# Kernel tuning notes

Measured on AMD Instinct MI355X. Metric: run time of the kernel, lower is better.

The kernel has to match this reference:

```python
import jax, jax.numpy as jnp
import numpy as np

N, D = 4096, 128  # seq length / feature dim of x is N; head dim is D

def setup_inputs() -> dict:
    key = jax.random.key(0)
    k1, k2 = jax.random.split(key)
    x = jax.random.normal(k1, (N, N), dtype=jnp.float32)
    # nn.Linear(N, 3*d): weight [3d, N], bias [3d]; scale weight like torch init
    W = jax.random.normal(k2, (3 * D, N), dtype=jnp.float32) / jnp.sqrt(jnp.float32(N))
    b = jnp.zeros((3 * D,), dtype=jnp.float32)
    return {"x": x, "W": W, "b": b}

def reference(x, W, b):
    # QKV projection: [N, 3d]
    qkv = x @ W.T + b
    Q, K, V = jnp.split(qkv, 3, axis=-1)  # each [N, d]
    # The blockwise online-softmax double loop computes exactly
    # softmax(Q K^T) V with NO 1/sqrt(d) scaling (faithful to source).
    S = Q @ K.T                 # [N, N]
    P = jax.nn.softmax(S, axis=-1)
    return P @ V                # [N, d]
```

## Files before the change

### kernel.cpp

```cpp
#include <hip/hip_runtime.h>
#include <cstdint>
#include <cstddef>

typedef _Float16 f16;
typedef f16 f16x8 __attribute__((ext_vector_type(8)));
typedef f16 f16x4 __attribute__((ext_vector_type(4)));
typedef float f32x4 __attribute__((ext_vector_type(4)));

#define SEQ 4096
#define DH 128
#define QKV_LD 384
#define LOG2E 1.44269504f

__device__ __forceinline__ float fast_exp2(float x) {
#if __has_builtin(__builtin_amdgcn_exp2f)
  return __builtin_amdgcn_exp2f(x);
#else
  return exp2f(x);
#endif
}

__device__ __forceinline__ void gl_lds16(const void* g, void* l) {
  __builtin_amdgcn_global_load_lds((const __attribute__((address_space(1))) void*)g,
                                   (__attribute__((address_space(3))) void*)l, 16, 0, 0);
}

__global__ __launch_bounds__(256) void cvt_kernel(const float4* __restrict__ src,
                                                  f16x4* __restrict__ dst) {
  int i = blockIdx.x * 256 + threadIdx.x;
  float4 v = src[i];
  f16x4 h; h[0] = (f16)v.x; h[1] = (f16)v.y; h[2] = (f16)v.z; h[3] = (f16)v.w;
  dst[i] = h;
}

template <int SPLITS>
__global__ __launch_bounds__(256, 3) void gemm_qkv(const f16* __restrict__ xh,
                                                   const f16* __restrict__ Wh,
                                                   f16* __restrict__ part) {
  __shared__ __align__(16) f16 Ax[128 * 64];
  __shared__ __align__(16) f16 Bx[128 * 64];
  const int m0 = blockIdx.x * 128;
  const int n0 = blockIdx.y * 128;
  const int split = blockIdx.z;
  const int kc = SEQ / SPLITS;
  const int k0 = split * kc;
  const int tid = threadIdx.x;
  const int lane = tid & 63, wave = tid >> 6;
  const int wr = (wave >> 1) * 64, wc = (wave & 1) * 64;
  const int l15 = lane & 15, quad = lane >> 4;

  f32x4 acc[4][4] = {};

  for (int kt = k0; kt < k0 + kc; kt += 64) {
#pragma unroll
    for (int r = 0; r < 4; ++r) {
      int c = r * 256 + tid;
      int row = c >> 3, ch = c & 7;
      gl_lds16(&xh[(size_t)(m0 + row) * SEQ + kt + ((ch ^ (row & 7)) << 3)],
               &Ax[(size_t)c << 3]);
    }
#pragma unroll
    for (int r = 0; r < 4; ++r) {
      int c = r * 256 + tid;
      int row = c >> 3, ch = c & 7;
      gl_lds16(&Wh[(size_t)(n0 + row) * SEQ + kt + ((ch ^ (row & 7)) << 3)],
               &Bx[(size_t)c << 3]);
    }
    __syncthreads();
#pragma unroll
    for (int ks = 0; ks < 2; ++ks) {
      f16x8 a[4], bb[4];
#pragma unroll
      for (int t = 0; t < 4; ++t) {
        int ar = wr + t * 16 + l15;
        int ac = (ks * 4 + quad) ^ (ar & 7);
        a[t] = *(const f16x8*)&Ax[ar * 64 + ac * 8];
        int br = wc + t * 16 + l15;
        int bc = (ks * 4 + quad) ^ (br & 7);
        bb[t] = *(const f16x8*)&Bx[br * 64 + bc * 8];
      }
#pragma unroll
      for (int mt = 0; mt < 4; ++mt)
#pragma unroll
        for (int nt = 0; nt < 4; ++nt)
          acc[mt][nt] = __builtin_amdgcn_mfma_f32_16x16x32_f16(a[mt], bb[nt], acc[mt][nt], 0, 0, 0);
    }
    __syncthreads();
  }

  f16* pw = part + (size_t)split * SEQ * QKV_LD;
#pragma unroll
  for (int mt = 0; mt < 4; ++mt) {
#pragma unroll
    for (int nt = 0; nt < 4; ++nt) {
      int col = n0 + wc + nt * 16 + l15;
      int rowbase = m0 + wr + mt * 16 + quad * 4;
#pragma unroll
      for (int rr = 0; rr < 4; ++rr)
        pw[(size_t)(rowbase + rr) * QKV_LD + col] = (f16)acc[mt][nt][rr];
    }
  }
}

template <int SPLITS>
__global__ __launch_bounds__(256) void reduce_qkv(const f16* __restrict__ part,
                                                  const float* __restrict__ bias,
                                                  f16* __restrict__ qkv) {
  int i = (blockIdx.x * 256 + threadIdx.x) * 8;
  float acc[8] = {};
#pragma unroll
  for (int s = 0; s < SPLITS; ++s) {
    f16x8 p = *(const f16x8*)&part[(size_t)s * SEQ * QKV_LD + i];
#pragma unroll
    for (int j = 0; j < 8; ++j) acc[j] += (float)p[j];
  }
  int col = i % QKV_LD;
  f16x8 o;
#pragma unroll
  for (int j = 0; j < 8; ++j) o[j] = (f16)(acc[j] + bias[col + j]);
  *(f16x8*)&qkv[i] = o;
}

__global__ __launch_bounds__(256) void transpose_v(const f16* __restrict__ qkv,
                                                   f16* __restrict__ Vt) {
  __shared__ __align__(16) f16 T[64][72];
  const int r0 = blockIdx.x * 64;
  const int c0 = blockIdx.y * 64;
  const int tid = threadIdx.x;
#pragma unroll
  for (int rep = 0; rep < 2; ++rep) {
    int idx = rep * 256 + tid;
    int row = idx >> 3, col = (idx & 7) * 8;
    *(f16x8*)&T[row][col] = *(const f16x8*)&qkv[(size_t)(r0 + row) * QKV_LD + 256 + c0 + col];
  }
  __syncthreads();
#pragma unroll
  for (int rep = 0; rep < 2; ++rep) {
    int idx = rep * 256 + tid;
    int cc = idx >> 3, rb = (idx & 7) * 8;
    f16x8 o;
#pragma unroll
    for (int j = 0; j < 8; ++j) o[j] = T[rb + j][cc];
    *(f16x8*)&Vt[(size_t)(c0 + cc) * SEQ + r0 + rb] = o;
  }
}

#define NSPLIT 16
#define KVRANGE (SEQ / NSPLIT)

__global__ __launch_bounds__(256, 3) void attn_partial(const f16* __restrict__ qkv,
                                                       const f16* __restrict__ Vt,
                                                       f16* __restrict__ Op,
                                                       float* __restrict__ ml) {
  __shared__ __align__(16) f16 Ks[64 * 128];
  __shared__ __align__(16) f16 Vs[128 * 64];
  __shared__ __align__(16) f16 Ps[4][16][72];

  const int q0 = blockIdx.x * 64;
  const int split = blockIdx.y;
  const int kv0 = split * KVRANGE;
  const int tid = threadIdx.x;
  const int lane = tid & 63, wave = tid >> 6;
  const int l15 = lane & 15, quad = lane >> 4;
  const int mbase = q0 + wave * 16;

  f16x8 qf[4];
#pragma unroll
  for (int ks = 0; ks < 4; ++ks) {
    f16x8 q = *(const f16x8*)&qkv[(size_t)(mbase + l15) * QKV_LD + ks * 32 + quad * 8];
    qf[ks] = q * (f16)LOG2E;
  }

  f32x4 oacc[8] = {};
  float mrow = -1e30f, lrow = 0.f;

  for (int it = 0; it < KVRANGE / 64; ++it) {
    const int k0 = kv0 + it * 64;
#pragma unroll
    for (int r = 0; r < 4; ++r) {
      int c = r * 256 + tid;
      int row = c >> 4, ch = c & 15;
      gl_lds16(&qkv[(size_t)(k0 + row) * QKV_LD + DH + ((ch ^ (row & 7)) << 3)],
               &Ks[(size_t)c << 3]);
    }
#pragma unroll
    for (int r = 0; r < 4; ++r) {
      int c = r * 256 + tid;
      int row = c >> 3, ch = c & 7;
      gl_lds16(&Vt[(size_t)row * SEQ + k0 + ((ch ^ (row & 7)) << 3)],
               &Vs[(size_t)c << 3]);
    }
    __syncthreads();

    f32x4 st[4] = {};
#pragma unroll
    for (int ks = 0; ks < 4; ++ks) {
      f16x8 kf[4];
#pragma unroll
      for (int kt = 0; kt < 4; ++kt) {
        int row = kt * 16 + l15;
        int ch = (ks * 4 + quad) ^ (row & 7);
        kf[kt] = *(const f16x8*)&Ks[row * 128 + ch * 8];
      }
#pragma unroll
      for (int kt = 0; kt < 4; ++kt)
        st[kt] = __builtin_amdgcn_mfma_f32_16x16x32_f16(kf[kt], qf[ks], st[kt], 0, 0, 0);
    }

    float v = -1e30f;
#pragma unroll
    for (int kt = 0; kt < 4; ++kt)
#pragma unroll
      for (int rr = 0; rr < 4; ++rr) v = fmaxf(v, st[kt][rr]);
    v = fmaxf(v, __shfl_xor(v, 16));
    v = fmaxf(v, __shfl_xor(v, 32));
    float mnew = fmaxf(mrow, v);
    float al = fast_exp2(mrow - mnew);
    mrow = mnew;
    float ls = 0.f;
#pragma unroll
    for (int kt = 0; kt < 4; ++kt) {
      f16x4 pk;
#pragma unroll
      for (int rr = 0; rr < 4; ++rr) {
        float p = fast_exp2(st[kt][rr] - mnew);
        ls += p;
        pk[rr] = (f16)p;
      }
      *(f16x4*)&Ps[wave][l15][kt * 16 + quad * 4] = pk;
    }
    ls += __shfl_xor(ls, 16);
    ls += __shfl_xor(ls, 32);
    lrow = lrow * al + ls;

    float alr[4];
#pragma unroll
    for (int rr = 0; rr < 4; ++rr) alr[rr] = __shfl(al, quad * 4 + rr);
#pragma unroll
    for (int dt = 0; dt < 8; ++dt)
#pragma unroll
      for (int rr = 0; rr < 4; ++rr) oacc[dt][rr] *= alr[rr];

#pragma unroll
    for (int kk = 0; kk < 2; ++kk) {
      f16x8 pf = *(const f16x8*)&Ps[wave][l15][kk * 32 + quad * 8];
#pragma unroll
      for (int dt = 0; dt < 8; ++dt) {
        int row = dt * 16 + l15;
        int ch = (kk * 4 + quad) ^ (row & 7);
        f16x8 vf = *(const f16x8*)&Vs[row * 64 + ch * 8];
        oacc[dt] = __builtin_amdgcn_mfma_f32_16x16x32_f16(pf, vf, oacc[dt], 0, 0, 0);
      }
    }
    __syncthreads();
  }

#pragma unroll
  for (int dt = 0; dt < 8; ++dt)
#pragma unroll
    for (int rr = 0; rr < 4; ++rr) {
      int row = mbase + quad * 4 + rr;
      Op[((size_t)split * SEQ + row) * DH + dt * 16 + l15] = (f16)oacc[dt][rr];
    }
  if (quad == 0) {
    int row = mbase + l15;
    ml[((size_t)split * SEQ + row) * 2 + 0] = mrow;
    ml[((size_t)split * SEQ + row) * 2 + 1] = lrow;
  }
}

__global__ __launch_bounds__(256) void combine_kernel(const f16* __restrict__ Op,
                                                      const float* __restrict__ ml,
                                                      float* __restrict__ out) {
  int idx = blockIdx.x * 256 + threadIdx.x;
  int row = idx >> 7;
  float ms[NSPLIT], ls[NSPLIT];
  float M = -1e30f;
#pragma unroll
  for (int s = 0; s < NSPLIT; ++s) {
    ms[s] = ml[((size_t)s * SEQ + row) * 2 + 0];
    ls[s] = ml[((size_t)s * SEQ + row) * 2 + 1];
    M = fmaxf(M, ms[s]);
  }
  float L = 0.f, o = 0.f;
#pragma unroll
  for (int s = 0; s < NSPLIT; ++s) {
    float w = fast_exp2(ms[s] - M);
    L += ls[s] * w;
    o += w * (float)Op[(size_t)s * SEQ * DH + idx];
  }
  out[idx] = o / L;
}

extern "C" void kernel_launch(void* const* d_in, const int* in_sizes, int n_in,
                              void* d_out, int out_size, void* d_ws, size_t ws_size,
                              hipStream_t stream) {
  const float* x = (const float*)d_in[0];
  const float* W = (const float*)d_in[1];
  const float* b = (const float*)d_in[2];
  float* out = (float*)d_out;
  char* ws = (char*)d_ws;

  f16*   Wh   = (f16*)(ws);
  f16*   xh   = (f16*)(ws + (3u << 20));
  f16*   qkv  = (f16*)(ws + (35u << 20));
  f16*   Vt   = (f16*)(ws + (38u << 20));
  float* ml   = (float*)(ws + (39u << 20));
  char*  scr  = ws + (40u << 20);
  f16*   part = (f16*)scr;
  f16*   Op   = (f16*)scr;

  cvt_kernel<<<(QKV_LD * SEQ / 4) / 256, 256, 0, stream>>>((const float4*)W, (f16x4*)Wh);
  cvt_kernel<<<((size_t)SEQ * SEQ / 4) / 256, 256, 0, stream>>>((const float4*)x, (f16x4*)xh);

  bool big = ws_size >= ((size_t)66u << 20);
  if (big) {
    gemm_qkv<8><<<dim3(SEQ / 128, 3, 8), 256, 0, stream>>>(xh, Wh, part);
    reduce_qkv<8><<<SEQ * QKV_LD / 8 / 256, 256, 0, stream>>>(part, b, qkv);
  } else {
    gemm_qkv<4><<<dim3(SEQ / 128, 3, 4), 256, 0, stream>>>(xh, Wh, part);
    reduce_qkv<4><<<SEQ * QKV_LD / 8 / 256, 256, 0, stream>>>(part, b, qkv);
  }
  transpose_v<<<dim3(SEQ / 64, DH / 64), 256, 0, stream>>>(qkv, Vt);
  attn_partial<<<dim3(SEQ / 64, NSPLIT), 256, 0, stream>>>(qkv, Vt, Op, ml);
  combine_kernel<<<(SEQ * DH) / 256, 256, 0, stream>>>(Op, ml, out);
}
```

Measured before the change: 160.7 us.

## Process two query tiles per wave in attention to reuse K/V fragments

Each wave in the attention kernel now handles 32 query rows (two 16-row MFMA tiles) instead of 16, so the block covers 128 queries and the grid halves along the query axis. Each K and V fragment read from LDS now feeds two MFMAs, and each block's K/V tile load serves twice as many queries. This cuts LDS reads and global K/V traffic per query. In exchange, register pressure roughly doubles for the accumulators, so launch bounds drop from 3 to 2 blocks per CU and fewer blocks are launched (512 instead of 1024), which may reduce latency hiding.

```diff
diff --git a/kernel.cpp b/kernel.cpp
--- a/kernel.cpp
+++ b/kernel.cpp
@@ -148,31 +148,34 @@
 #define NSPLIT 16
 #define KVRANGE (SEQ / NSPLIT)
 
-__global__ __launch_bounds__(256, 3) void attn_partial(const f16* __restrict__ qkv,
+__global__ __launch_bounds__(256, 2) void attn_partial(const f16* __restrict__ qkv,
                                                        const f16* __restrict__ Vt,
                                                        f16* __restrict__ Op,
                                                        float* __restrict__ ml) {
   __shared__ __align__(16) f16 Ks[64 * 128];
   __shared__ __align__(16) f16 Vs[128 * 64];
-  __shared__ __align__(16) f16 Ps[4][16][72];
-
-  const int q0 = blockIdx.x * 64;
+  __shared__ __align__(16) f16 Ps[4][32][72];
+
+  const int q0 = blockIdx.x * 128;
   const int split = blockIdx.y;
   const int kv0 = split * KVRANGE;
   const int tid = threadIdx.x;
   const int lane = tid & 63, wave = tid >> 6;
   const int l15 = lane & 15, quad = lane >> 4;
-  const int mbase = q0 + wave * 16;
-
-  f16x8 qf[4];
-#pragma unroll
-  for (int ks = 0; ks < 4; ++ks) {
-    f16x8 q = *(const f16x8*)&qkv[(size_t)(mbase + l15) * QKV_LD + ks * 32 + quad * 8];
-    qf[ks] = q * (f16)LOG2E;
-  }
-
-  f32x4 oacc[8] = {};
-  float mrow = -1e30f, lrow = 0.f;
+  const int mbase = q0 + wave * 32;
+
+  f16x8 qf[2][4];
+#pragma unroll
+  for (int mt = 0; mt < 2; ++mt)
+#pragma unroll
+    for (int ks = 0; ks < 4; ++ks) {
+      f16x8 q = *(const f16x8*)&qkv[(size_t)(mbase + mt * 16 + l15) * QKV_LD + ks * 32 + quad * 8];
+      qf[mt][ks] = q * (f16)LOG2E;
+    }
+
+  f32x4 oacc[2][8] = {};
+  float mrow[2] = {-1e30f, -1e30f};
+  float lrow[2] = {0.f, 0.f};
 
   for (int it = 0; it < KVRANGE / 64; ++it) {
     const int k0 = kv0 + it * 64;
@@ -192,7 +195,7 @@
     }
     __syncthreads();
 
-    f32x4 st[4] = {};
+    f32x4 st[4][2] = {};
 #pragma unroll
     for (int ks = 0; ks < 4; ++ks) {
       f16x8 kf[4];
@@ -204,68 +207,88 @@
       }
 #pragma unroll
       for (int kt = 0; kt < 4; ++kt)
-        st[kt] = __builtin_amdgcn_mfma_f32_16x16x32_f16(kf[kt], qf[ks], st[kt], 0, 0, 0);
-    }
-
-    float v = -1e30f;
-#pragma unroll
-    for (int kt = 0; kt < 4; ++kt)
-#pragma unroll
-      for (int rr = 0; rr < 4; ++rr) v = fmaxf(v, st[kt][rr]);
-    v = fmaxf(v, __shfl_xor(v, 16));
-    v = fmaxf(v, __shfl_xor(v, 32));
-    float mnew = fmaxf(mrow, v);
-    float al = fast_exp2(mrow - mnew);
-    mrow = mnew;
-    float ls = 0.f;
-#pragma unroll
-    for (int kt = 0; kt < 4; ++kt) {
-      f16x4 pk;
-#pragma unroll
-      for (int rr = 0; rr < 4; ++rr) {
-        float p = fast_exp2(st[kt][rr] - mnew);
-        ls += p;
-        pk[rr] = (f16)p;
-      }
-      *(f16x4*)&Ps[wave][l15][kt * 16 + quad * 4] = pk;
-    }
-    ls += __shfl_xor(ls, 16);
-    ls += __shfl_xor(ls, 32);
-    lrow = lrow * al + ls;
-
-    float alr[4];
-#pragma unroll
-    for (int rr = 0; rr < 4; ++rr) alr[rr] = __shfl(al, quad * 4 + rr);
-#pragma unroll
-    for (int dt = 0; dt < 8; ++dt)
-#pragma unroll
-      for (int rr = 0; rr < 4; ++rr) oacc[dt][rr] *= alr[rr];
+#pragma unroll
+        for (int mt = 0; mt < 2; ++mt)
+          st[kt][mt] = __builtin_amdgcn_mfma_f32_16x16x32_f16(kf[kt], qf[mt][ks], st[kt][mt], 0, 0, 0);
+    }
+
+    float al[2];
+#pragma unroll
+    for (int mt = 0; mt < 2; ++mt) {
+      float v = -1e30f;
+#pragma unroll
+      for (int kt = 0; kt < 4; ++kt)
+#pragma unroll
+        for (int rr = 0; rr < 4; ++rr) v = fmaxf(v, st[kt][mt][rr]);
+      v = fmaxf(v, __shfl_xor(v, 16));
+      v = fmaxf(v, __shfl_xor(v, 32));
+      float mnew = fmaxf(mrow[mt], v);
+      al[mt] = fast_exp2(mrow[mt] - mnew);
+      mrow[mt] = mnew;
+      float ls = 0.f;
+#pragma unroll
+      for (int kt = 0; kt < 4; ++kt) {
+        f16x4 pk;
+#pragma unroll
+        for (int rr = 0; rr < 4; ++rr) {
+          float p = fast_exp2(st[kt][mt][rr] - mnew);
+          ls += p;
+          pk[rr] = (f16)p;
+        }
+        *(f16x4*)&Ps[wave][mt * 16 + l15][kt * 16 + quad * 4] = pk;
+      }
+      ls += __shfl_xor(ls, 16);
+      ls += __shfl_xor(ls, 32);
+      lrow[mt] = lrow[mt] * al[mt] + ls;
+    }
+
+    float alr[2][4];
+#pragma unroll
+    for (int mt = 0; mt < 2; ++mt)
+#pragma unroll
+      for (int rr = 0; rr < 4; ++rr) alr[mt][rr] = __shfl(al[mt], quad * 4 + rr);
+#pragma unroll
+    for (int mt = 0; mt < 2; ++mt)
+#pragma unroll
+      for (int dt = 0; dt < 8; ++dt)
+#pragma unroll
+        for (int rr = 0; rr < 4; ++rr) oacc[mt][dt][rr] *= alr[mt][rr];
 
 #pragma unroll
     for (int kk = 0; kk < 2; ++kk) {
-      f16x8 pf = *(const f16x8*)&Ps[wave][l15][kk * 32 + quad * 8];
+      f16x8 pf[2];
+#pragma unroll
+      for (int mt = 0; mt < 2; ++mt)
+        pf[mt] = *(const f16x8*)&Ps[wave][mt * 16 + l15][kk * 32 + quad * 8];
 #pragma unroll
       for (int dt = 0; dt < 8; ++dt) {
         int row = dt * 16 + l15;
         int ch = (kk * 4 + quad) ^ (row & 7);
         f16x8 vf = *(const f16x8*)&Vs[row * 64 + ch * 8];
-        oacc[dt] = __builtin_amdgcn_mfma_f32_16x16x32_f16(pf, vf, oacc[dt], 0, 0, 0);
+#pragma unroll
+        for (int mt = 0; mt < 2; ++mt)
+          oacc[mt][dt] = __builtin_amdgcn_mfma_f32_16x16x32_f16(pf[mt], vf, oacc[mt][dt], 0, 0, 0);
       }
     }
     __syncthreads();
   }
 
 #pragma unroll
-  for (int dt = 0; dt < 8; ++dt)
-#pragma unroll
-    for (int rr = 0; rr < 4; ++rr) {
-      int row = mbase + quad * 4 + rr;
-      Op[((size_t)split * SEQ + row) * DH + dt * 16 + l15] = (f16)oacc[dt][rr];
-    }
+  for (int mt = 0; mt < 2; ++mt)
+#pragma unroll
+    for (int dt = 0; dt < 8; ++dt)
+#pragma unroll
+      for (int rr = 0; rr < 4; ++rr) {
+        int row = mbase + mt * 16 + quad * 4 + rr;
+        Op[((size_t)split * SEQ + row) * DH + dt * 16 + l15] = (f16)oacc[mt][dt][rr];
+      }
   if (quad == 0) {
-    int row = mbase + l15;
-    ml[((size_t)split * SEQ + row) * 2 + 0] = mrow;
-    ml[((size_t)split * SEQ + row) * 2 + 1] = lrow;
+#pragma unroll
+    for (int mt = 0; mt < 2; ++mt) {
+      int row = mbase + mt * 16 + l15;
+      ml[((size_t)split * SEQ + row) * 2 + 0] = mrow[mt];
+      ml[((size_t)split * SEQ + row) * 2 + 1] = lrow[mt];
+    }
   }
 }
 
@@ -322,6 +345,6 @@
     reduce_qkv<4><<<SEQ * QKV_LD / 8 / 256, 256, 0, stream>>>(part, b, qkv);
   }
   transpose_v<<<dim3(SEQ / 64, DH / 64), 256, 0, stream>>>(qkv, Vt);
-  attn_partial<<<dim3(SEQ / 64, NSPLIT), 256, 0, stream>>>(qkv, Vt, Op, ml);
+  attn_partial<<<dim3(SEQ / 128, NSPLIT), 256, 0, stream>>>(qkv, Vt, Op, ml);
   combine_kernel<<<(SEQ * DH) / 256, 256, 0, stream>>>(Op, ml, out);
 }
```

New measurement: 158.9 us. No clear change (-1.1%).
